# Kernel optimization log

Measured on AMD Instinct MI355X. Metric: run time of the kernel, lower is better.

Reference implementation:

```python
import jax, jax.numpy as jnp
import numpy as np

B, C, H, W = 64, 3, 512, 512
KSIZE = 13
EPS = 8.0
IDENTITY_OFFSET = 4.0
DEFORM_OFFSET = (2.0 + IDENTITY_OFFSET / (W - 1)) / 2.0
SCALE_X = IDENTITY_OFFSET / (W - 1)
SCALE_Y = IDENTITY_OFFSET / (H - 1)


def setup_inputs() -> dict:
    key = jax.random.key(0)
    k1, k2 = jax.random.split(key)
    image = jax.random.uniform(k1, (B, C, H, W), dtype=jnp.float32)
    prim_grid = jax.random.normal(k2, (B, 2, H, W), dtype=jnp.float32) * 0.01
    return {"image": image, "prim_grid": prim_grid}


def _samp_iden():
    seq = jnp.arange(-(W - 1), W, 2, dtype=jnp.float32) / (W - 1)
    gx = jnp.broadcast_to(seq[None, :], (H, W))
    gy = gx.T
    return jnp.stack([gx, gy], axis=0)[None]  # [1,2,H,W]


def _gaussian_blur(x, ksize):
    sigma = ksize * 0.15 + 0.35
    half = (ksize - 1) * 0.5
    t = jnp.linspace(-half, half, ksize)
    pdf = jnp.exp(-0.5 * (t / sigma) ** 2)
    k1 = pdf / pdf.sum()
    k2d = jnp.outer(k1, k1)
    p = ksize // 2
    xp = jnp.pad(x, ((0, 0), (0, 0), (p, p), (p, p)), mode='reflect')
    kernel = jnp.broadcast_to(k2d[None, None], (2, 1, ksize, ksize))
    return jax.lax.conv_general_dilated(
        xp, kernel, window_strides=(1, 1), padding='VALID',
        feature_group_count=2, dimension_numbers=('NCHW', 'OIHW', 'NCHW'))


def _samp2accu(samp):
    # conv_transpose with [1,-1] kernel + crop == first-difference with zero prepend
    s = samp + DEFORM_OFFSET
    ax = jnp.diff(s[:, 0:1], axis=3, prepend=jnp.zeros_like(s[:, 0:1, :, :1])) / SCALE_X
    ay = jnp.diff(s[:, 1:2], axis=2, prepend=jnp.zeros_like(s[:, 1:2, :1, :])) / SCALE_Y
    return jnp.concatenate([ax, ay], axis=1)


def _accu2samp(accu):
    # conv_transpose with full-ones kernel + crop == cumulative sum
    sx = jnp.cumsum(accu[:, 0:1] * SCALE_X, axis=3)
    sy = jnp.cumsum(accu[:, 1:2] * SCALE_Y, axis=2)
    return jnp.concatenate([sx, sy], axis=1) - DEFORM_OFFSET


def _grid_sample(image, grid):
    # image [B,C,H,W], grid [B,H,W,2] xy in [-1,1], bilinear, align_corners=True, zeros pad
    gx = (grid[..., 0] + 1.0) * 0.5 * (W - 1)
    gy = (grid[..., 1] + 1.0) * 0.5 * (H - 1)
    x0 = jnp.floor(gx)
    y0 = jnp.floor(gy)
    wx = gx - x0
    wy = gy - y0
    x0i = x0.astype(jnp.int32)
    x1i = x0i + 1
    y0i = y0.astype(jnp.int32)
    y1i = y0i + 1

    def gather(img, yi, xi):
        valid = ((xi >= 0) & (xi < W) & (yi >= 0) & (yi < H)).astype(img.dtype)
        xc = jnp.clip(xi, 0, W - 1)
        yc = jnp.clip(yi, 0, H - 1)
        return img[:, yc, xc] * valid[None]  # [C,H,W]

    def per_b(img, y0i, y1i, x0i, x1i, wx, wy):
        v00 = gather(img, y0i, x0i)
        v01 = gather(img, y0i, x1i)
        v10 = gather(img, y1i, x0i)
        v11 = gather(img, y1i, x1i)
        return (v00 * (1 - wx) * (1 - wy) + v01 * wx * (1 - wy)
                + v10 * (1 - wx) * wy + v11 * wx * wy)

    return jax.vmap(per_b)(image, y0i, y1i, x0i, x1i, wx, wy)


def _forward_grid(prim_grid):
    iden = _samp_iden()
    p = _gaussian_blur(prim_grid, KSIZE)
    accu = jnp.maximum(_samp2accu(p + iden), 0.0)          # accu_clip (relu)
    p = _accu2samp(accu) - iden
    bound = (2.0 / W) * EPS
    p = jnp.clip(p, -bound, bound)                          # prim_clip
    samp = jnp.clip(p + iden, -1.0, 1.0)                    # samp_clip (hardtanh)
    return samp


def reference(image, prim_grid):
    samp = _forward_grid(prim_grid)
    grid = jnp.transpose(samp, (0, 2, 3, 1))  # [B,H,W,2]
    return _grid_sample(image, grid)
```

## Files before the change

### kernel.cpp

```cpp
#include <hip/hip_runtime.h>
#include <math.h>

#define HH 512
#define WW 512
#define NB 64
#define HW (HH*WW)

struct GaussK { float k[13]; };

__device__ __forceinline__ float idenv(int i) {
    return (float)(2*i - (WW-1)) / (float)(WW-1);
}

#define DEF_OFF ((float)((2.0 + 4.0/511.0)/2.0))
#define BOUND   ((float)(2.0/512.0*8.0))

typedef float vf2 __attribute__((ext_vector_type(2), aligned(4)));

__global__ void __launch_bounds__(256) k_hblur(const float* __restrict__ prim, float* __restrict__ out, GaussK gk) {
    int idx = blockIdx.x*256 + threadIdx.x;
    int w4 = idx & 127;
    int h  = (idx >> 7) & (HH-1);
    int b  = idx >> 16;
    const float* src = prim + ((size_t)b*2 + 1)*HW + (size_t)h*WW;
    float t[16];
    if (w4 >= 2 && w4 <= 125) {
        const float4* s4 = (const float4*)(src) + (w4 - 2);
        float flat[20];
        #pragma unroll
        for (int j = 0; j < 5; ++j) {
            float4 v = s4[j];
            flat[4*j+0] = v.x; flat[4*j+1] = v.y; flat[4*j+2] = v.z; flat[4*j+3] = v.w;
        }
        #pragma unroll
        for (int j = 0; j < 16; ++j) t[j] = flat[j+2];
    } else {
        #pragma unroll
        for (int j = 0; j < 16; ++j) {
            int x = w4*4 - 6 + j;
            x = x < 0 ? -x : (x > WW-1 ? 2*(WW-1) - x : x);
            t[j] = src[x];
        }
    }
    float4 o;
    float* op = (float*)&o;
    #pragma unroll
    for (int j = 0; j < 4; ++j) {
        float acc = 0.f;
        #pragma unroll
        for (int i = 0; i < 13; ++i) acc = fmaf(gk.k[i], t[j+i], acc);
        op[j] = acc;
    }
    ((float4*)(out + ((size_t)b*3 + 1)*HW))[(size_t)h*128 + w4] = o;
}

__global__ void __launch_bounds__(256) k_xscan(const float* __restrict__ prim, float* __restrict__ out, GaussK gk) {
    int lane = threadIdx.x & 63;
    int bid  = (int)blockIdx.x;
    int work = (bid & 7)*1024 + (bid >> 3);
    int gw   = work*4 + (threadIdx.x >> 6);
    int b    = gw >> 9;
    int h    = gw & (HH-1);
    const float4* src = (const float4*)(prim + (size_t)b*2*HW);
    float* plane0 = out + (size_t)b*3*HW + (size_t)h*WW;

    int rows[13];
    #pragma unroll
    for (int i = 0; i < 13; ++i) {
        int r = h - 6 + i;
        rows[i] = r < 0 ? -r : (r > HH-1 ? 2*(HH-1) - r : r);
    }

    float a[8];
    #pragma unroll
    for (int t = 0; t < 2; ++t) {
        int g = 2*lane + t;
        float4 acc = {0.f,0.f,0.f,0.f};
        #pragma unroll
        for (int i = 0; i < 13; ++i) {
            float4 v = src[(size_t)rows[i]*128 + g];
            acc.x = fmaf(gk.k[i], v.x, acc.x);
            acc.y = fmaf(gk.k[i], v.y, acc.y);
            acc.z = fmaf(gk.k[i], v.z, acc.z);
            acc.w = fmaf(gk.k[i], v.w, acc.w);
        }
        a[4*t+0] = acc.x; a[4*t+1] = acc.y; a[4*t+2] = acc.z; a[4*t+3] = acc.w;
    }

    float win[21];
    #pragma unroll
    for (int i = 0; i < 7; ++i) {
        float v = __shfl_up(a[i+1], 1, 64);
        win[i] = (lane == 0) ? a[7-i] : v;
    }
    #pragma unroll
    for (int i = 0; i < 8; ++i) win[7+i] = a[i];
    #pragma unroll
    for (int i = 15; i < 21; ++i) {
        float v = __shfl_down(a[i-15], 1, 64);
        win[i] = (lane == 63) ? a[21-i] : v;
    }

    float s[9];
    #pragma unroll
    for (int j = 0; j < 9; ++j) {
        float acc = 0.f;
        #pragma unroll
        for (int i = 0; i < 13; ++i) acc = fmaf(gk.k[i], win[j+i], acc);
        s[j] = acc + idenv(8*lane - 1 + j) + DEF_OFF;
    }
    if (lane == 0) s[0] = 0.f;

    float qs[8], q = 0.f;
    #pragma unroll
    for (int j = 1; j < 9; ++j) { q += fmaxf(s[j] - s[j-1], 0.f); qs[j-1] = q; }
    float inc = q;
    #pragma unroll
    for (int d = 1; d < 64; d <<= 1) {
        float t = __shfl_up(inc, d, 64);
        if (lane >= d) inc += t;
    }
    float excl = inc - q;

    float4 g0, g1;
    float* gp0 = (float*)&g0;
    float* gp1 = (float*)&g1;
    #pragma unroll
    for (int j = 0; j < 8; ++j) {
        int wcol = lane*8 + j;
        float sx = excl + qs[j];
        float p = sx - DEF_OFF - idenv(wcol);
        p = fminf(fmaxf(p, -BOUND), BOUND);
        float g = p + idenv(wcol);
        g = fminf(fmaxf(g, -1.f), 1.f);
        if (j < 4) gp0[j] = g; else gp1[j-4] = g;
    }
    *(float4*)(plane0 + lane*8)     = g0;
    *(float4*)(plane0 + lane*8 + 4) = g1;
}

__global__ void __launch_bounds__(1024) k_yscan(float* __restrict__ out, GaussK gk) {
    __shared__ float segsum[16][64];
    int b    = blockIdx.x >> 3;
    int wt   = blockIdx.x & 7;
    int lane = threadIdx.x & 63;
    int ws   = threadIdx.x >> 6;
    int w    = wt*64 + lane;
    const float* p1 = out + ((size_t)b*3 + 1)*HW + w;
    float*       p2 = out + ((size_t)b*3 + 2)*HW + w;
    int r0 = ws*32;

    float v[45];
    #pragma unroll
    for (int j = 0; j < 45; ++j) {
        int r = r0 - 7 + j;
        r = r < 0 ? -r : (r > HH-1 ? 2*(HH-1) - r : r);
        v[j] = p1[(size_t)r*WW];
    }

    float sprev;
    if (ws == 0) {
        sprev = 0.f;
    } else {
        float acc = 0.f;
        #pragma unroll
        for (int i = 0; i < 13; ++i) acc = fmaf(gk.k[i], v[i], acc);
        sprev = acc + idenv(r0 - 1) + DEF_OFF;
    }

    float q[32];
    float run = 0.f;
    #pragma unroll
    for (int n = 0; n < 32; ++n) {
        float acc = 0.f;
        #pragma unroll
        for (int i = 0; i < 13; ++i) acc = fmaf(gk.k[i], v[n+1+i], acc);
        float s = acc + idenv(r0 + n) + DEF_OFF;
        run += fmaxf(s - sprev, 0.f);
        q[n] = run;
        sprev = s;
    }
    segsum[ws][lane] = run;
    __syncthreads();
    float off = 0.f;
    for (int k = 0; k < ws; ++k) off += segsum[k][lane];

    #pragma unroll
    for (int n = 0; n < 32; ++n) {
        int h = r0 + n;
        float p = off + q[n] - DEF_OFF - idenv(h);
        p = fminf(fmaxf(p, -BOUND), BOUND);
        float g = p + idenv(h);
        g = fminf(fmaxf(g, -1.f), 1.f);
        p2[(size_t)h*WW] = g;
    }
}

__global__ void __launch_bounds__(256) k_sample(const float* __restrict__ image, float* __restrict__ out) {
    int bid  = (int)blockIdx.x;
    int work = (bid & 7)*4096 + (bid >> 3);
    int idx  = work*256 + threadIdx.x;
    int w  = idx & (WW-1);
    int h  = (idx >> 9) & (HH-1);
    int b0 = idx >> 18;
    int off = h*WW + w;

    #pragma unroll
    for (int u = 0; u < 2; ++u) {
        int b = b0 + 32*u;
        float* ob = out + (size_t)b*3*HW;
        const float* ib = image + (size_t)b*3*HW;
        float gx = ob[off];
        float gy = ob[2*HW + off];
        float fx = (gx + 1.f) * 0.5f * (float)(WW-1);
        float fy = (gy + 1.f) * 0.5f * (float)(HH-1);
        float x0f = floorf(fx), y0f = floorf(fy);
        float wx = fx - x0f, wy = fy - y0f;
        int x0 = (int)x0f, y0 = (int)y0f;
        int y1 = y0 + 1; if (y1 > HH-1) y1 = HH-1;
        bool sh = x0 > WW-2;
        int xb = sh ? WW-2 : x0;
        size_t r0 = (size_t)y0*WW + xb;
        size_t r1 = (size_t)y1*WW + xb;
        float w11 = wx*wy;
        float w01 = wx - w11;
        float w10 = wy - w11;
        float w00 = 1.f - wx - wy + w11;
        #pragma unroll
        for (int c = 0; c < 3; ++c) {
            const float* ip = ib + (size_t)c*HW;
            vf2 t  = *(const vf2*)(ip + r0);
            vf2 bo = *(const vf2*)(ip + r1);
            float a00 = sh ? t.y  : t.x;
            float a10 = sh ? bo.y : bo.x;
            float r = a00*w00 + t.y*w01 + a10*w10 + bo.y*w11;
            __builtin_nontemporal_store(r, ob + (size_t)c*HW + off);
        }
    }
}

extern "C" void kernel_launch(void* const* d_in, const int* in_sizes, int n_in,
                              void* d_out, int out_size, void* d_ws, size_t ws_size,
                              hipStream_t stream) {
    const float* image = (const float*)d_in[0];
    const float* prim  = (const float*)d_in[1];
    float* out = (float*)d_out;

    GaussK gk;
    {
        double sigma = 13.0*0.15 + 0.35;
        double pdf[13], sum = 0.0;
        for (int i = 0; i < 13; ++i) {
            double t = (double)(i - 6);
            pdf[i] = exp(-0.5*(t/sigma)*(t/sigma));
            sum += pdf[i];
        }
        for (int i = 0; i < 13; ++i) gk.k[i] = (float)(pdf[i]/sum);
    }

    int nQuad = NB*HH*WW/4;
    k_hblur <<<nQuad/256,      256, 0, stream>>>(prim, out, gk);
    k_xscan <<<NB*HH/4,        256, 0, stream>>>(prim, out, gk);
    k_yscan <<<NB*8,          1024, 0, stream>>>(out, gk);
    k_sample<<<NB*HH*WW/2/256, 256, 0, stream>>>(image, out);
}
```

Measured before the change: 271.1 us.

## Fuse horizontal blur and x-scan into one kernel processing two rows per wave

Merges the horizontal-blur kernel for channel 1 and the x-scan kernel for channel 0 into a single prep kernel, removing one launch. Each wave now handles two adjacent rows, reading 14 input rows once to build both vertical-blur accumulators instead of reading 13 rows per output row. The channel-1 horizontal blur uses wave shuffles with reflect handling at the edges instead of per-thread reloads of neighbouring columns. The cost is higher register pressure per thread and fewer waves in the grid.

```diff
diff --git a/kernel.cpp b/kernel.cpp
--- a/kernel.cpp
+++ b/kernel.cpp
@@ -17,76 +17,30 @@
 
 typedef float vf2 __attribute__((ext_vector_type(2), aligned(4)));
 
-__global__ void __launch_bounds__(256) k_hblur(const float* __restrict__ prim, float* __restrict__ out, GaussK gk) {
-    int idx = blockIdx.x*256 + threadIdx.x;
-    int w4 = idx & 127;
-    int h  = (idx >> 7) & (HH-1);
-    int b  = idx >> 16;
-    const float* src = prim + ((size_t)b*2 + 1)*HW + (size_t)h*WW;
-    float t[16];
-    if (w4 >= 2 && w4 <= 125) {
-        const float4* s4 = (const float4*)(src) + (w4 - 2);
-        float flat[20];
-        #pragma unroll
-        for (int j = 0; j < 5; ++j) {
-            float4 v = s4[j];
-            flat[4*j+0] = v.x; flat[4*j+1] = v.y; flat[4*j+2] = v.z; flat[4*j+3] = v.w;
-        }
-        #pragma unroll
-        for (int j = 0; j < 16; ++j) t[j] = flat[j+2];
-    } else {
-        #pragma unroll
-        for (int j = 0; j < 16; ++j) {
-            int x = w4*4 - 6 + j;
-            x = x < 0 ? -x : (x > WW-1 ? 2*(WW-1) - x : x);
-            t[j] = src[x];
-        }
-    }
-    float4 o;
-    float* op = (float*)&o;
-    #pragma unroll
-    for (int j = 0; j < 4; ++j) {
-        float acc = 0.f;
-        #pragma unroll
-        for (int i = 0; i < 13; ++i) acc = fmaf(gk.k[i], t[j+i], acc);
-        op[j] = acc;
-    }
-    ((float4*)(out + ((size_t)b*3 + 1)*HW))[(size_t)h*128 + w4] = o;
-}
-
-__global__ void __launch_bounds__(256) k_xscan(const float* __restrict__ prim, float* __restrict__ out, GaussK gk) {
-    int lane = threadIdx.x & 63;
-    int bid  = (int)blockIdx.x;
-    int work = (bid & 7)*1024 + (bid >> 3);
-    int gw   = work*4 + (threadIdx.x >> 6);
-    int b    = gw >> 9;
-    int h    = gw & (HH-1);
-    const float4* src = (const float4*)(prim + (size_t)b*2*HW);
-    float* plane0 = out + (size_t)b*3*HW + (size_t)h*WW;
-
-    int rows[13];
-    #pragma unroll
-    for (int i = 0; i < 13; ++i) {
-        int r = h - 6 + i;
-        rows[i] = r < 0 ? -r : (r > HH-1 ? 2*(HH-1) - r : r);
-    }
-
-    float a[8];
-    #pragma unroll
-    for (int t = 0; t < 2; ++t) {
-        int g = 2*lane + t;
-        float4 acc = {0.f,0.f,0.f,0.f};
-        #pragma unroll
-        for (int i = 0; i < 13; ++i) {
-            float4 v = src[(size_t)rows[i]*128 + g];
-            acc.x = fmaf(gk.k[i], v.x, acc.x);
-            acc.y = fmaf(gk.k[i], v.y, acc.y);
-            acc.z = fmaf(gk.k[i], v.z, acc.z);
-            acc.w = fmaf(gk.k[i], v.w, acc.w);
-        }
-        a[4*t+0] = acc.x; a[4*t+1] = acc.y; a[4*t+2] = acc.z; a[4*t+3] = acc.w;
-    }
-
+__device__ __forceinline__ void hconv_row(const float (&a)[8], int lane, const GaussK& gk, float (&o)[8]) {
+    float win[20];
+    #pragma unroll
+    for (int i = 0; i < 6; ++i) {
+        float v = __shfl_up(a[i+2], 1, 64);
+        win[i] = (lane == 0) ? a[6-i] : v;
+    }
+    #pragma unroll
+    for (int i = 6; i < 14; ++i) win[i] = a[i-6];
+    #pragma unroll
+    for (int i = 14; i < 20; ++i) {
+        float v = __shfl_down(a[i-14], 1, 64);
+        win[i] = (lane == 63) ? a[20-i] : v;
+    }
+    #pragma unroll
+    for (int j = 0; j < 8; ++j) {
+        float acc = 0.f;
+        #pragma unroll
+        for (int i = 0; i < 13; ++i) acc = fmaf(gk.k[i], win[j+i], acc);
+        o[j] = acc;
+    }
+}
+
+__device__ __forceinline__ void xscan_row(const float (&a)[8], int lane, const GaussK& gk, float* row0) {
     float win[21];
     #pragma unroll
     for (int i = 0; i < 7; ++i) {
@@ -100,7 +54,6 @@
         float v = __shfl_down(a[i-15], 1, 64);
         win[i] = (lane == 63) ? a[21-i] : v;
     }
-
     float s[9];
     #pragma unroll
     for (int j = 0; j < 9; ++j) {
@@ -135,8 +88,57 @@
         g = fminf(fmaxf(g, -1.f), 1.f);
         if (j < 4) gp0[j] = g; else gp1[j-4] = g;
     }
-    *(float4*)(plane0 + lane*8)     = g0;
-    *(float4*)(plane0 + lane*8 + 4) = g1;
+    *(float4*)(row0 + lane*8)     = g0;
+    *(float4*)(row0 + lane*8 + 4) = g1;
+}
+
+__global__ void __launch_bounds__(256) k_prep(const float* __restrict__ prim, float* __restrict__ out, GaussK gk) {
+    int lane = threadIdx.x & 63;
+    int bid  = (int)blockIdx.x;
+    int work = (bid & 7)*512 + (bid >> 3);
+    int gw   = work*4 + ((int)threadIdx.x >> 6);
+    int b    = gw >> 8;
+    int h0   = (gw & 255)*2;
+
+    const float4* src0 = (const float4*)(prim + (size_t)b*2*HW);
+    const float*  src1 = prim + ((size_t)b*2 + 1)*HW;
+    float* plane0 = out + (size_t)b*3*HW;
+    float* plane1 = out + ((size_t)b*3 + 1)*HW;
+
+    float a0[8] = {0,0,0,0,0,0,0,0};
+    float a1[8] = {0,0,0,0,0,0,0,0};
+    #pragma unroll
+    for (int i = 0; i < 14; ++i) {
+        int r = h0 - 6 + i;
+        r = r < 0 ? -r : (r > HH-1 ? 2*(HH-1) - r : r);
+        float4 u0 = src0[(size_t)r*128 + 2*lane];
+        float4 u1 = src0[(size_t)r*128 + 2*lane + 1];
+        float vv[8] = {u0.x,u0.y,u0.z,u0.w,u1.x,u1.y,u1.z,u1.w};
+        if (i < 13) {
+            #pragma unroll
+            for (int j = 0; j < 8; ++j) a0[j] = fmaf(gk.k[i], vv[j], a0[j]);
+        }
+        if (i >= 1) {
+            #pragma unroll
+            for (int j = 0; j < 8; ++j) a1[j] = fmaf(gk.k[i-1], vv[j], a1[j]);
+        }
+    }
+
+    #pragma unroll
+    for (int r = 0; r < 2; ++r) {
+        const float4* c4 = (const float4*)(src1 + (size_t)(h0+r)*WW);
+        float4 u0 = c4[2*lane];
+        float4 u1 = c4[2*lane + 1];
+        float c[8] = {u0.x,u0.y,u0.z,u0.w,u1.x,u1.y,u1.z,u1.w};
+        float o[8];
+        hconv_row(c, lane, gk, o);
+        float* row1 = plane1 + (size_t)(h0+r)*WW;
+        *(float4*)(row1 + lane*8)     = make_float4(o[0],o[1],o[2],o[3]);
+        *(float4*)(row1 + lane*8 + 4) = make_float4(o[4],o[5],o[6],o[7]);
+    }
+
+    xscan_row(a0, lane, gk, plane0 + (size_t)h0*WW);
+    xscan_row(a1, lane, gk, plane0 + (size_t)(h0+1)*WW);
 }
 
 __global__ void __launch_bounds__(1024) k_yscan(float* __restrict__ out, GaussK gk) {
@@ -258,9 +260,7 @@
         for (int i = 0; i < 13; ++i) gk.k[i] = (float)(pdf[i]/sum);
     }
 
-    int nQuad = NB*HH*WW/4;
-    k_hblur <<<nQuad/256,      256, 0, stream>>>(prim, out, gk);
-    k_xscan <<<NB*HH/4,        256, 0, stream>>>(prim, out, gk);
+    k_prep  <<<4096,           256, 0, stream>>>(prim, out, gk);
     k_yscan <<<NB*8,          1024, 0, stream>>>(out, gk);
     k_sample<<<NB*HH*WW/2/256, 256, 0, stream>>>(image, out);
 }
```

Result: faster. 251.5 us (-7.2%).
